# Performance work log

Measured on AMD Instinct MI355X. Metric: run time of the kernel, lower is better.

The kernel has to match this reference:

```python
import jax, jax.numpy as jnp
import numpy as np


def lstm_cell(carry, x, Wx, Wh, b):
    # carry = (h, c), x: [B, E]; standard fused-gate LSTM
    h, c = carry
    z = x @ Wx + h @ Wh + b  # [B, 4U]
    i, f, g, o = jnp.split(z, 4, axis=-1)
    c = jax.nn.sigmoid(f) * c + jax.nn.sigmoid(i) * jnp.tanh(g)
    h = jax.nn.sigmoid(o) * jnp.tanh(c)
    return (h, c)


def run_lstm(xs, Wx, Wh, b, units):
    # xs: [T, B, E] -> final hidden state [B, U]
    B = xs.shape[1]
    init = (jnp.zeros((B, units), xs.dtype), jnp.zeros((B, units), xs.dtype))
    def step(carry, x):
        carry = lstm_cell(carry, x, Wx, Wh, b)
        return carry, None
    (h, _), _ = jax.lax.scan(step, init, xs)
    return h


def setup_inputs() -> dict:
    key = jax.random.key(0)
    ks = jax.random.split(key, 12)
    B, T, V, E, U = 64, 512, 50000, 256, 512
    s = lambda *d: 1.0 / np.sqrt(d[0])
    return {
        "sentence": jax.random.randint(ks[0], (B, T), 0, V, dtype=jnp.int32),
        "emb": jax.random.normal(ks[1], (V, E), jnp.float32) * 0.02,
        "Wx_f": jax.random.normal(ks[2], (E, 4 * U), jnp.float32) * s(E),
        "Wh_f": jax.random.normal(ks[3], (U, 4 * U), jnp.float32) * s(U),
        "b_f": jnp.zeros((4 * U,), jnp.float32),
        "Wx_b": jax.random.normal(ks[4], (E, 4 * U), jnp.float32) * s(E),
        "Wh_b": jax.random.normal(ks[5], (U, 4 * U), jnp.float32) * s(U),
        "b_b": jnp.zeros((4 * U,), jnp.float32),
        "W1": jax.random.normal(ks[6], (2 * U, 64), jnp.float32) * s(2 * U),
        "b1": jnp.zeros((64,), jnp.float32),
        "W2": jax.random.normal(ks[7], (64, 1), jnp.float32) * s(64),
        "b2": jnp.zeros((1,), jnp.float32),
    }


def reference(sentence, emb, Wx_f, Wh_f, b_f, Wx_b, Wh_b, b_b, W1, b1, W2, b2):
    U = Wh_f.shape[0]
    x = emb[sentence]                      # [B, T, E]
    xs = jnp.swapaxes(x, 0, 1)             # [T, B, E]
    h_fwd = run_lstm(xs, Wx_f, Wh_f, b_f, U)           # forward direction
    h_bwd = run_lstm(xs[::-1], Wx_b, Wh_b, b_b, U)     # backward direction
    h = jnp.concatenate([h_fwd, h_bwd], axis=1)        # [B, 2U]
    hidden = h @ W1 + b1                    # Dense(64), linear
    return jax.nn.sigmoid(hidden @ W2 + b2) # Dense(1, sigmoid)
```

## Files before the change

kernel.cpp:

```cpp
#include <hip/hip_runtime.h>
#include <hip/hip_bf16.h>

typedef __bf16 bf16x8 __attribute__((ext_vector_type(8)));
typedef float f32x4 __attribute__((ext_vector_type(4)));
typedef unsigned int u32;
typedef unsigned short u16;
typedef unsigned long long u64;

#define T_ 512
#define E_ 256
#define U_ 512

static const size_t WS_XS = 0;
static const size_t WS_W2 = (size_t)16 << 20;
static const size_t WS_HP = WS_W2 + 6291456;
static const size_t WS_HF = WS_HP + 524288;

__device__ __forceinline__ float fsigm(float x) { return 1.f / (1.f + __expf(-x)); }
__device__ __forceinline__ float ftanh(float x) {
  float e = __expf(2.f * fabsf(x));
  float r = 1.f - 2.f / (e + 1.f);
  return copysignf(r, x);
}

__global__ void embed_swz_kernel(const int* __restrict__ sent,
                                 const float* __restrict__ emb,
                                 __bf16* __restrict__ xs_g) {
  int id = blockIdx.x * 256 + threadIdx.x;
  int gx = id & 31;
  int b  = (id >> 5) & 63;
  int t  = id >> 11;
  int idx = sent[b * T_ + t];
  const float* src = emb + (size_t)idx * E_ + gx * 8;
  bf16x8 v;
#pragma unroll
  for (int j = 0; j < 8; ++j) v[j] = (__bf16)src[j];
  int gs = gx ^ (b & 7);
  *(bf16x8*)(xs_g + (size_t)(t * 64 + b) * E_ + gs * 8) = v;
}

__global__ void __launch_bounds__(256)
wprep_kernel(const float* __restrict__ Wx_f, const float* __restrict__ Wh_f,
             const float* __restrict__ Wx_b, const float* __restrict__ Wh_b,
             __bf16* __restrict__ w2, u32* __restrict__ hpub) {
  int bid = blockIdx.x;
  int tid = threadIdx.x;
  {
    int zid = bid * 256 + tid;
    if (zid < 131072) hpub[zid] = 0u;
  }
  int jg = bid % 6;
  int wv = (bid / 6) & 7;
  int us = (bid / 48) & 15;
  int d  = bid / 768;
  int j    = jg * 4 + (tid >> 6);
  int lane = tid & 63;
  int c    = wv * 16 + (lane & 15);
  int ul   = c >> 2, gate = c & 3;
  int n    = gate * 512 + us * 32 + ul;
  int k0   = j * 32 + (lane >> 4) * 8;
  const float* Wx = d ? Wx_b : Wx_f;
  const float* Wh = d ? Wh_b : Wh_f;
  bf16x8 v;
#pragma unroll
  for (int e = 0; e < 8; ++e) {
    int k = k0 + e;
    float f = (k < 256) ? Wx[(size_t)k * 2048 + n] : Wh[(size_t)(k - 256) * 2048 + n];
    v[e] = (__bf16)f;
  }
  size_t og = ((size_t)((d * 16 + us) * 8 + wv) * 24 + j) * 64 + lane;
  *(bf16x8*)(w2 + og * 8) = v;
}

__global__ void __launch_bounds__(512)
lstm_main(const __bf16* __restrict__ xs_g, const __bf16* __restrict__ w2,
          u32* __restrict__ hpub, float* __restrict__ hfin,
          const float* __restrict__ b_f, const float* __restrict__ b_b) {
  __shared__ __align__(16) __bf16 xbuf[2][16 * 256];
  __shared__ __align__(16) __bf16 hbuf[16 * 512];

  const int wg   = blockIdx.x;
  const int dir  = wg >> 6;
  const int sl   = wg & 63;
  const int us   = sl >> 2;
  const int q    = sl & 3;
  const int tid  = threadIdx.x;
  const int wv   = tid >> 6;
  const int lane = tid & 63;
  const int bq_l = lane & 15;
  const int kq   = lane >> 4;
  const int bsw  = bq_l & 7;
  const int ul_own = wv * 4 + kq;
  const int u_own  = us * 32 + ul_own;
  const int b_own  = q * 16 + bq_l;

  bf16x8 wfrag[24];
  {
    const bf16x8* wp = (const bf16x8*)w2 +
                       ((size_t)((dir * 16 + us) * 8 + wv) * 24) * 64 + lane;
#pragma unroll
    for (int j = 0; j < 24; ++j) wfrag[j] = wp[j * 64];
  }

  const float* bias = dir ? b_b : b_f;
  const float bi  = bias[u_own];
  const float bff = bias[512 + u_own];
  const float bg  = bias[1024 + u_own];
  const float bo  = bias[1536 + u_own];
  float c_st = 0.f;

  u32* const pw0 = hpub + ((size_t)(dir * 2 + 0) * 64 + q * 16 + us) * 512 + wv * 64 + lane;
  u32* const pw1 = pw0 + 32768;

  const int us_p  = 2 * wv + (lane >> 5);
  const int lane5 = lane & 31;
  const u64* const cs0 = (const u64*)(hpub + ((size_t)(dir * 2 + 0) * 64 + q * 16 + us_p) * 512) + lane5;
  const u64* const cs1 = cs0 + 16384;
  const int cc = lane5 >> 3;
  const int cb0 = 2 * (lane5 & 7);
  const int cb1 = cb0 + 1;
  int cd0[8], cd1[8];
#pragma unroll
  for (int j = 0; j < 8; ++j) {
    int u = us_p * 32 + j * 4 + cc;
    int g = u >> 3;
    cd0[j] = cb0 * 1024 + ((g ^ (cb0 & 7)) << 4) + ((u & 7) << 1);
    cd1[j] = cb1 * 1024 + ((g ^ (cb1 & 7)) << 4) + ((u & 7) << 1);
  }

  {
    int t0 = dir ? (T_ - 1) : 0;
    const uint4* xsrc = (const uint4*)(xs_g + ((size_t)t0 * 64 + q * 16) * 256);
    ((uint4*)xbuf[0])[tid] = xsrc[tid];
  }
  __syncthreads();

  for (int t = 0;; ++t) {
    const bool lastt = (t == T_ - 1);
    u64 v[8];
    const u64* csrc = (t & 1) ? cs1 : cs0;
    if (t > 0) {
#pragma unroll
      for (int j = 0; j < 8; ++j)
        v[j] = __hip_atomic_load(csrc + j * 32, __ATOMIC_RELAXED, __HIP_MEMORY_SCOPE_AGENT);
    }
    uint4 xg;
    if (!lastt) {
      const int teff = dir ? (T_ - 2 - t) : (t + 1);
      xg = ((const uint4*)(xs_g + ((size_t)teff * 64 + q * 16) * 256))[tid];
    }

    f32x4 acc0 = {0.f, 0.f, 0.f, 0.f};
    f32x4 acc1 = {0.f, 0.f, 0.f, 0.f};
    const __bf16* xb = xbuf[t & 1];
#pragma unroll
    for (int j = 0; j < 8; ++j) {
      int g = j * 4 + kq;
      bf16x8 a = *(const bf16x8*)(xb + bq_l * 256 + ((g ^ bsw) << 3));
      if (j & 1) acc1 = __builtin_amdgcn_mfma_f32_16x16x32_bf16(wfrag[j], a, acc1, 0, 0, 0);
      else       acc0 = __builtin_amdgcn_mfma_f32_16x16x32_bf16(wfrag[j], a, acc0, 0, 0, 0);
    }

    if (t > 0) {
      const u32 ep = (u32)t;
      for (;;) {
        u32 bad = 0;
#pragma unroll
        for (int j = 0; j < 8; ++j)
          bad |= ((u32)v[j] ^ ep) | ((u32)(v[j] >> 32) ^ ep);
        bad &= 0xFFFFu;
        if (!__any((int)bad)) break;
        __builtin_amdgcn_s_sleep(1);
#pragma unroll
        for (int j = 0; j < 8; ++j)
          v[j] = __hip_atomic_load(csrc + j * 32, __ATOMIC_RELAXED, __HIP_MEMORY_SCOPE_AGENT);
      }
#pragma unroll
      for (int j = 0; j < 8; ++j) {
        *(u16*)((char*)hbuf + cd0[j]) = (u16)(v[j] >> 16);
        *(u16*)((char*)hbuf + cd1[j]) = (u16)(v[j] >> 48);
      }
      __syncthreads();
#pragma unroll
      for (int j = 0; j < 16; ++j) {
        int g = j * 4 + kq;
        bf16x8 a = *(const bf16x8*)(hbuf + bq_l * 512 + ((g ^ bsw) << 3));
        if (j & 1) acc1 = __builtin_amdgcn_mfma_f32_16x16x32_bf16(wfrag[8 + j], a, acc1, 0, 0, 0);
        else       acc0 = __builtin_amdgcn_mfma_f32_16x16x32_bf16(wfrag[8 + j], a, acc0, 0, 0, 0);
      }
    }

    const float zi = acc0[0] + acc1[0] + bi;
    const float zf = acc0[1] + acc1[1] + bff;
    const float zg = acc0[2] + acc1[2] + bg;
    const float zo = acc0[3] + acc1[3] + bo;
    c_st = fsigm(zf) * c_st + fsigm(zi) * ftanh(zg);
    const float hv = fsigm(zo) * ftanh(c_st);

    if (lastt) {
      hfin[(size_t)dir * 32768 + b_own * 512 + u_own] = hv;
      break;
    }

    {
      union { __bf16 h; u16 s; } cv;
      cv.h = (__bf16)hv;
      u32 word = ((u32)cv.s << 16) | (u32)(t + 1);
      __hip_atomic_store(((t + 1) & 1) ? pw1 : pw0, word, __ATOMIC_RELAXED,
                         __HIP_MEMORY_SCOPE_AGENT);
    }
    ((uint4*)xbuf[(t + 1) & 1])[tid] = xg;
    __syncthreads();
  }
}

__global__ void __launch_bounds__(1024)
dense_kernel(const float* __restrict__ hfin, const float* __restrict__ W1,
             const float* __restrict__ b1, const float* __restrict__ W2,
             const float* __restrict__ b2, float* __restrict__ out) {
  __shared__ float hid[64][64];
  const int t = threadIdx.x;
  const int b = t >> 4;
  const int jg = t & 15;
  float a0 = b1[jg * 4 + 0], a1 = b1[jg * 4 + 1], a2 = b1[jg * 4 + 2], a3 = b1[jg * 4 + 3];
#pragma unroll 8
  for (int k = 0; k < 1024; ++k) {
    const float hv = hfin[(size_t)(k >> 9) * 32768 + b * 512 + (k & 511)];
    const float4 w = *(const float4*)(W1 + (size_t)k * 64 + jg * 4);
    a0 += hv * w.x; a1 += hv * w.y; a2 += hv * w.z; a3 += hv * w.w;
  }
  hid[b][jg * 4 + 0] = a0; hid[b][jg * 4 + 1] = a1;
  hid[b][jg * 4 + 2] = a2; hid[b][jg * 4 + 3] = a3;
  __syncthreads();
  if (t < 64) {
    float l = b2[0];
#pragma unroll 8
    for (int j = 0; j < 64; ++j) l += hid[t][j] * W2[j];
    out[t] = 1.f / (1.f + __expf(-l));
  }
}

extern "C" void kernel_launch(void* const* d_in, const int* in_sizes, int n_in,
                              void* d_out, int out_size, void* d_ws, size_t ws_size,
                              hipStream_t stream) {
  const int*   sent = (const int*)d_in[0];
  const float* emb  = (const float*)d_in[1];
  const float* Wx_f = (const float*)d_in[2];
  const float* Wh_f = (const float*)d_in[3];
  const float* b_f  = (const float*)d_in[4];
  const float* Wx_b = (const float*)d_in[5];
  const float* Wh_b = (const float*)d_in[6];
  const float* b_b  = (const float*)d_in[7];
  const float* W1   = (const float*)d_in[8];
  const float* b1   = (const float*)d_in[9];
  const float* W2   = (const float*)d_in[10];
  const float* b2   = (const float*)d_in[11];
  float* out = (float*)d_out;

  char* ws = (char*)d_ws;
  __bf16* xs_g = (__bf16*)(ws + WS_XS);
  __bf16* w2   = (__bf16*)(ws + WS_W2);
  u32*    hpub = (u32*)(ws + WS_HP);
  float*  hfin = (float*)(ws + WS_HF);

  hipLaunchKernelGGL(embed_swz_kernel, dim3(4096), dim3(256), 0, stream, sent, emb, xs_g);
  hipLaunchKernelGGL(wprep_kernel, dim3(1536), dim3(256), 0, stream,
                     Wx_f, Wh_f, Wx_b, Wh_b, w2, hpub);

  void* args[] = {(void*)&xs_g, (void*)&w2, (void*)&hpub, (void*)&hfin,
                  (void*)&b_f, (void*)&b_b};
  hipLaunchCooperativeKernel((void*)lstm_main, dim3(128), dim3(512), args, 0, stream);

  hipLaunchKernelGGL(dense_kernel, dim3(1), dim3(1024), 0, stream,
                     hfin, W1, b1, W2, b2, out);
}
```

Measured before the change: 1.308 ms.

## Split LSTM recurrence over 256 smaller workgroups and hoist input projection

Re-partitions the persistent cooperative LSTM kernel from 128 workgroups of 512 threads to 256 workgroups of 256 threads, so each workgroup owns 16 hidden units instead of 32. The weight pre-layout and the h-publish buffer indexing change to match. The x-projection MFMAs for the next step now run right after the barrier, off the critical path that waits on h. The h gather is rewritten to pack four bf16 values per 64-bit LDS store. In exchange, each workgroup waits on more cross-workgroup flags per step, and twice as many workgroups take part in the grid-wide handshake.

```diff
diff --git a/kernel.cpp b/kernel.cpp
--- a/kernel.cpp
+++ b/kernel.cpp
@@ -50,14 +50,14 @@
     if (zid < 131072) hpub[zid] = 0u;
   }
   int jg = bid % 6;
-  int wv = (bid / 6) & 7;
-  int us = (bid / 48) & 15;
+  int wv = (bid / 6) & 3;
+  int us = (bid / 24) & 31;
   int d  = bid / 768;
   int j    = jg * 4 + (tid >> 6);
   int lane = tid & 63;
   int c    = wv * 16 + (lane & 15);
   int ul   = c >> 2, gate = c & 3;
-  int n    = gate * 512 + us * 32 + ul;
+  int n    = gate * 512 + us * 16 + ul;
   int k0   = j * 32 + (lane >> 4) * 8;
   const float* Wx = d ? Wx_b : Wx_f;
   const float* Wh = d ? Wh_b : Wh_f;
@@ -68,11 +68,11 @@
     float f = (k < 256) ? Wx[(size_t)k * 2048 + n] : Wh[(size_t)(k - 256) * 2048 + n];
     v[e] = (__bf16)f;
   }
-  size_t og = ((size_t)((d * 16 + us) * 8 + wv) * 24 + j) * 64 + lane;
+  size_t og = ((size_t)((d * 32 + us) * 4 + wv) * 24 + j) * 64 + lane;
   *(bf16x8*)(w2 + og * 8) = v;
 }
 
-__global__ void __launch_bounds__(512)
+__global__ void __launch_bounds__(256)
 lstm_main(const __bf16* __restrict__ xs_g, const __bf16* __restrict__ w2,
           u32* __restrict__ hpub, float* __restrict__ hfin,
           const float* __restrict__ b_f, const float* __restrict__ b_b) {
@@ -80,8 +80,8 @@
   __shared__ __align__(16) __bf16 hbuf[16 * 512];
 
   const int wg   = blockIdx.x;
-  const int dir  = wg >> 6;
-  const int sl   = wg & 63;
+  const int dir  = wg >> 7;
+  const int sl   = wg & 127;
   const int us   = sl >> 2;
   const int q    = sl & 3;
   const int tid  = threadIdx.x;
@@ -91,13 +91,13 @@
   const int kq   = lane >> 4;
   const int bsw  = bq_l & 7;
   const int ul_own = wv * 4 + kq;
-  const int u_own  = us * 32 + ul_own;
+  const int u_own  = us * 16 + ul_own;
   const int b_own  = q * 16 + bq_l;
 
   bf16x8 wfrag[24];
   {
     const bf16x8* wp = (const bf16x8*)w2 +
-                       ((size_t)((dir * 16 + us) * 8 + wv) * 24) * 64 + lane;
+                       ((size_t)((dir * 32 + us) * 4 + wv) * 24) * 64 + lane;
 #pragma unroll
     for (int j = 0; j < 24; ++j) wfrag[j] = wp[j * 64];
   }
@@ -109,76 +109,95 @@
   const float bo  = bias[1536 + u_own];
   float c_st = 0.f;
 
-  u32* const pw0 = hpub + ((size_t)(dir * 2 + 0) * 64 + q * 16 + us) * 512 + wv * 64 + lane;
+  u32* const pw0 = hpub + ((size_t)(dir * 2 + 0) * 4 + q) * 8192 + us * 256 + wv * 64 + lane;
   u32* const pw1 = pw0 + 32768;
 
-  const int us_p  = 2 * wv + (lane >> 5);
-  const int lane5 = lane & 31;
-  const u64* const cs0 = (const u64*)(hpub + ((size_t)(dir * 2 + 0) * 64 + q * 16 + us_p) * 512) + lane5;
-  const u64* const cs1 = cs0 + 16384;
-  const int cc = lane5 >> 3;
-  const int cb0 = 2 * (lane5 & 7);
-  const int cb1 = cb0 + 1;
-  int cd0[8], cd1[8];
-#pragma unroll
-  for (int j = 0; j < 8; ++j) {
-    int u = us_p * 32 + j * 4 + cc;
-    int g = u >> 3;
-    cd0[j] = cb0 * 1024 + ((g ^ (cb0 & 7)) << 4) + ((u & 7) << 1);
-    cd1[j] = cb1 * 1024 + ((g ^ (cb1 & 7)) << 4) + ((u & 7) << 1);
+  const int b2  = tid & 7;
+  const int u0  = ((tid >> 3) & 3) * 4;
+  const int ush = tid >> 5;
+  const u64* const cb = (const u64*)hpub + ((size_t)(dir * 2 + 0) * 4 + q) * 4096;
+  int cde[4], cdo[4];
+#pragma unroll
+  for (int J = 0; J < 4; ++J) {
+    int us_p = ush + 8 * J;
+    int ga   = us_p * 2 + (u0 >> 3);
+    int off  = (u0 & 7) * 2;
+    int b0   = 2 * b2, b1 = 2 * b2 + 1;
+    cde[J] = b0 * 1024 + ((ga ^ (b0 & 7)) << 4) + off;
+    cdo[J] = b1 * 1024 + ((ga ^ (b1 & 7)) << 4) + off;
   }
 
   {
     int t0 = dir ? (T_ - 1) : 0;
     const uint4* xsrc = (const uint4*)(xs_g + ((size_t)t0 * 64 + q * 16) * 256);
     ((uint4*)xbuf[0])[tid] = xsrc[tid];
+    ((uint4*)xbuf[0])[tid + 256] = xsrc[tid + 256];
   }
   __syncthreads();
+
+  f32x4 xacc0 = {0.f, 0.f, 0.f, 0.f};
+  f32x4 xacc1 = {0.f, 0.f, 0.f, 0.f};
+#pragma unroll
+  for (int j = 0; j < 8; ++j) {
+    int g = j * 4 + kq;
+    bf16x8 a = *(const bf16x8*)(xbuf[0] + bq_l * 256 + ((g ^ bsw) << 3));
+    if (j & 1) xacc1 = __builtin_amdgcn_mfma_f32_16x16x32_bf16(wfrag[j], a, xacc1, 0, 0, 0);
+    else       xacc0 = __builtin_amdgcn_mfma_f32_16x16x32_bf16(wfrag[j], a, xacc0, 0, 0, 0);
+  }
 
   for (int t = 0;; ++t) {
     const bool lastt = (t == T_ - 1);
-    u64 v[8];
-    const u64* csrc = (t & 1) ? cs1 : cs0;
+    u64 v[16];
+    const u64* csrc = cb + (size_t)(t & 1) * 16384;
     if (t > 0) {
 #pragma unroll
-      for (int j = 0; j < 8; ++j)
-        v[j] = __hip_atomic_load(csrc + j * 32, __ATOMIC_RELAXED, __HIP_MEMORY_SCOPE_AGENT);
-    }
-    uint4 xg;
+      for (int J = 0; J < 4; ++J)
+#pragma unroll
+        for (int du = 0; du < 4; ++du)
+          v[J * 4 + du] = __hip_atomic_load(
+              csrc + (ush + 8 * J) * 128 + (u0 + du) * 8 + b2,
+              __ATOMIC_RELAXED, __HIP_MEMORY_SCOPE_AGENT);
+    }
+    uint4 xg0, xg1;
     if (!lastt) {
       const int teff = dir ? (T_ - 2 - t) : (t + 1);
-      xg = ((const uint4*)(xs_g + ((size_t)teff * 64 + q * 16) * 256))[tid];
-    }
-
-    f32x4 acc0 = {0.f, 0.f, 0.f, 0.f};
-    f32x4 acc1 = {0.f, 0.f, 0.f, 0.f};
-    const __bf16* xb = xbuf[t & 1];
-#pragma unroll
-    for (int j = 0; j < 8; ++j) {
-      int g = j * 4 + kq;
-      bf16x8 a = *(const bf16x8*)(xb + bq_l * 256 + ((g ^ bsw) << 3));
-      if (j & 1) acc1 = __builtin_amdgcn_mfma_f32_16x16x32_bf16(wfrag[j], a, acc1, 0, 0, 0);
-      else       acc0 = __builtin_amdgcn_mfma_f32_16x16x32_bf16(wfrag[j], a, acc0, 0, 0, 0);
-    }
+      const uint4* xsrc = (const uint4*)(xs_g + ((size_t)teff * 64 + q * 16) * 256);
+      xg0 = xsrc[tid];
+      xg1 = xsrc[tid + 256];
+    }
+
+    f32x4 acc0 = xacc0;
+    f32x4 acc1 = xacc1;
 
     if (t > 0) {
       const u32 ep = (u32)t;
       for (;;) {
         u32 bad = 0;
 #pragma unroll
-        for (int j = 0; j < 8; ++j)
+        for (int j = 0; j < 16; ++j)
           bad |= ((u32)v[j] ^ ep) | ((u32)(v[j] >> 32) ^ ep);
         bad &= 0xFFFFu;
         if (!__any((int)bad)) break;
         __builtin_amdgcn_s_sleep(1);
 #pragma unroll
-        for (int j = 0; j < 8; ++j)
-          v[j] = __hip_atomic_load(csrc + j * 32, __ATOMIC_RELAXED, __HIP_MEMORY_SCOPE_AGENT);
+        for (int J = 0; J < 4; ++J)
+#pragma unroll
+          for (int du = 0; du < 4; ++du)
+            v[J * 4 + du] = __hip_atomic_load(
+                csrc + (ush + 8 * J) * 128 + (u0 + du) * 8 + b2,
+                __ATOMIC_RELAXED, __HIP_MEMORY_SCOPE_AGENT);
       }
 #pragma unroll
-      for (int j = 0; j < 8; ++j) {
-        *(u16*)((char*)hbuf + cd0[j]) = (u16)(v[j] >> 16);
-        *(u16*)((char*)hbuf + cd1[j]) = (u16)(v[j] >> 48);
+      for (int J = 0; J < 4; ++J) {
+        u64 we = 0, wo = 0;
+#pragma unroll
+        for (int du = 0; du < 4; ++du) {
+          u64 x = v[J * 4 + du];
+          we |= (u64)((u32)(x >> 16) & 0xFFFFu) << (16 * du);
+          wo |= (u64)((u32)(x >> 48) & 0xFFFFu) << (16 * du);
+        }
+        *(u64*)((char*)hbuf + cde[J]) = we;
+        *(u64*)((char*)hbuf + cdo[J]) = wo;
       }
       __syncthreads();
 #pragma unroll
@@ -209,8 +228,23 @@
       __hip_atomic_store(((t + 1) & 1) ? pw1 : pw0, word, __ATOMIC_RELAXED,
                          __HIP_MEMORY_SCOPE_AGENT);
     }
-    ((uint4*)xbuf[(t + 1) & 1])[tid] = xg;
+    {
+      uint4* xdst = (uint4*)xbuf[(t + 1) & 1];
+      xdst[tid] = xg0;
+      xdst[tid + 256] = xg1;
+    }
     __syncthreads();
+
+    xacc0 = (f32x4){0.f, 0.f, 0.f, 0.f};
+    xacc1 = (f32x4){0.f, 0.f, 0.f, 0.f};
+    const __bf16* xb = xbuf[(t + 1) & 1];
+#pragma unroll
+    for (int j = 0; j < 8; ++j) {
+      int g = j * 4 + kq;
+      bf16x8 a = *(const bf16x8*)(xb + bq_l * 256 + ((g ^ bsw) << 3));
+      if (j & 1) xacc1 = __builtin_amdgcn_mfma_f32_16x16x32_bf16(wfrag[j], a, xacc1, 0, 0, 0);
+      else       xacc0 = __builtin_amdgcn_mfma_f32_16x16x32_bf16(wfrag[j], a, xacc0, 0, 0, 0);
+    }
   }
 }
 
@@ -269,7 +303,7 @@
 
   void* args[] = {(void*)&xs_g, (void*)&w2, (void*)&hpub, (void*)&hfin,
                   (void*)&b_f, (void*)&b_b};
-  hipLaunchCooperativeKernel((void*)lstm_main, dim3(128), dim3(512), args, 0, stream);
+  hipLaunchCooperativeKernel((void*)lstm_main, dim3(256), dim3(256), args, 0, stream);
 
   hipLaunchKernelGGL(dense_kernel, dim3(1), dim3(1024), 0, stream,
                      hfin, W1, b1, W2, b2, out);
```

Result: slower. 1.358 ms (+3.8%).

## Halve LSTM workgroups, give each wave two column tiles, split h exchange into halves

Applied to the files above, without the earlier changes.

Each workgroup now owns 64 hidden units instead of 32, so the cooperative launch drops from 128 to 64 workgroups and every wave keeps 48 weight fragments in registers across two column tiles. The h exchange is restructured: loads are packed into 64-bit LDS stores, and the recurrent matmul is split into two halves, so work on the first half of h can start before the second half has been published. The aim is to cut the cross-workgroup synchronisation cost and overlap communication with MFMA work. The cost is higher register pressure (48 fragments plus more accumulators) under launch_bounds(512,2), a risk of spilling, and more serial compute per step.

```diff
diff --git a/kernel.cpp b/kernel.cpp
--- a/kernel.cpp
+++ b/kernel.cpp
@@ -50,14 +50,17 @@
     if (zid < 131072) hpub[zid] = 0u;
   }
   int jg = bid % 6;
-  int wv = (bid / 6) & 7;
-  int us = (bid / 48) & 15;
+  int ct = (bid / 6) & 1;
+  int wv = (bid / 12) & 7;
+  int us = (bid / 96) & 7;
   int d  = bid / 768;
   int j    = jg * 4 + (tid >> 6);
   int lane = tid & 63;
-  int c    = wv * 16 + (lane & 15);
-  int ul   = c >> 2, gate = c & 3;
-  int n    = gate * 512 + us * 32 + ul;
+  int r    = lane & 15;
+  int tile = wv * 2 + ct;
+  int ul   = tile * 4 + (r >> 2);
+  int gate = r & 3;
+  int n    = gate * 512 + us * 64 + ul;
   int k0   = j * 32 + (lane >> 4) * 8;
   const float* Wx = d ? Wx_b : Wx_f;
   const float* Wh = d ? Wh_b : Wh_f;
@@ -68,11 +71,11 @@
     float f = (k < 256) ? Wx[(size_t)k * 2048 + n] : Wh[(size_t)(k - 256) * 2048 + n];
     v[e] = (__bf16)f;
   }
-  size_t og = ((size_t)((d * 16 + us) * 8 + wv) * 24 + j) * 64 + lane;
+  size_t og = ((size_t)(((d * 8 + us) * 8 + wv) * 2 + ct) * 24 + j) * 64 + lane;
   *(bf16x8*)(w2 + og * 8) = v;
 }
 
-__global__ void __launch_bounds__(512)
+__global__ void __launch_bounds__(512, 2)
 lstm_main(const __bf16* __restrict__ xs_g, const __bf16* __restrict__ w2,
           u32* __restrict__ hpub, float* __restrict__ hfin,
           const float* __restrict__ b_f, const float* __restrict__ b_b) {
@@ -80,8 +83,8 @@
   __shared__ __align__(16) __bf16 hbuf[16 * 512];
 
   const int wg   = blockIdx.x;
-  const int dir  = wg >> 6;
-  const int sl   = wg & 63;
+  const int dir  = wg >> 5;
+  const int sl   = wg & 31;
   const int us   = sl >> 2;
   const int q    = sl & 3;
   const int tid  = threadIdx.x;
@@ -90,42 +93,46 @@
   const int bq_l = lane & 15;
   const int kq   = lane >> 4;
   const int bsw  = bq_l & 7;
-  const int ul_own = wv * 4 + kq;
-  const int u_own  = us * 32 + ul_own;
   const int b_own  = q * 16 + bq_l;
 
-  bf16x8 wfrag[24];
+  bf16x8 wfrag[48];
   {
     const bf16x8* wp = (const bf16x8*)w2 +
-                       ((size_t)((dir * 16 + us) * 8 + wv) * 24) * 64 + lane;
-#pragma unroll
-    for (int j = 0; j < 24; ++j) wfrag[j] = wp[j * 64];
+                       ((size_t)((dir * 8 + us) * 8 + wv) * 48) * 64 + lane;
+#pragma unroll
+    for (int j = 0; j < 48; ++j) wfrag[j] = wp[j * 64];
   }
 
   const float* bias = dir ? b_b : b_f;
-  const float bi  = bias[u_own];
-  const float bff = bias[512 + u_own];
-  const float bg  = bias[1024 + u_own];
-  const float bo  = bias[1536 + u_own];
-  float c_st = 0.f;
-
-  u32* const pw0 = hpub + ((size_t)(dir * 2 + 0) * 64 + q * 16 + us) * 512 + wv * 64 + lane;
-  u32* const pw1 = pw0 + 32768;
-
-  const int us_p  = 2 * wv + (lane >> 5);
-  const int lane5 = lane & 31;
-  const u64* const cs0 = (const u64*)(hpub + ((size_t)(dir * 2 + 0) * 64 + q * 16 + us_p) * 512) + lane5;
-  const u64* const cs1 = cs0 + 16384;
-  const int cc = lane5 >> 3;
-  const int cb0 = 2 * (lane5 & 7);
-  const int cb1 = cb0 + 1;
-  int cd0[8], cd1[8];
-#pragma unroll
-  for (int j = 0; j < 8; ++j) {
-    int u = us_p * 32 + j * 4 + cc;
-    int g = u >> 3;
-    cd0[j] = cb0 * 1024 + ((g ^ (cb0 & 7)) << 4) + ((u & 7) << 1);
-    cd1[j] = cb1 * 1024 + ((g ^ (cb1 & 7)) << 4) + ((u & 7) << 1);
+  float bi[2], bff[2], bg[2], bo[2], c_st[2];
+  int u_own[2];
+#pragma unroll
+  for (int ct = 0; ct < 2; ++ct) {
+    u_own[ct] = us * 64 + (wv * 2 + ct) * 4 + kq;
+    bi[ct]  = bias[u_own[ct]];
+    bff[ct] = bias[512 + u_own[ct]];
+    bg[ct]  = bias[1024 + u_own[ct]];
+    bo[ct]  = bias[1536 + u_own[ct]];
+    c_st[ct] = 0.f;
+  }
+
+  u32* const pw0 = hpub + ((size_t)(dir * 2 + 0) * 4 + q) * 8192 +
+                   us * 1024 + wv * 128 + lane;
+
+  const int ph   = tid >> 7;
+  const int inr  = tid & 127;
+  const int b2   = inr & 7;
+  const int u0g  = inr >> 3;
+  const int u0   = u0g * 4;
+  const u64* const cb = (const u64*)hpub + ((size_t)(dir * 2 + 0) * 4 + q) * 4096;
+  const int be = 2 * b2, bo_ = 2 * b2 + 1;
+  int cde[2], cdo[2];
+#pragma unroll
+  for (int H = 0; H < 2; ++H) {
+    int g0  = (H * 4 + ph) * 8 + (u0g >> 1);
+    int off = (u0g & 1) * 8;
+    cde[H] = be  * 1024 + ((g0 ^ (be  & 7)) << 4) + off;
+    cdo[H] = bo_ * 1024 + ((g0 ^ (bo_ & 7)) << 4) + off;
   }
 
   {
@@ -138,11 +145,15 @@
   for (int t = 0;; ++t) {
     const bool lastt = (t == T_ - 1);
     u64 v[8];
-    const u64* csrc = (t & 1) ? cs1 : cs0;
+    const u64* csrc = cb + (size_t)(t & 1) * 16384;
     if (t > 0) {
 #pragma unroll
-      for (int j = 0; j < 8; ++j)
-        v[j] = __hip_atomic_load(csrc + j * 32, __ATOMIC_RELAXED, __HIP_MEMORY_SCOPE_AGENT);
+      for (int H = 0; H < 2; ++H)
+#pragma unroll
+        for (int du = 0; du < 4; ++du)
+          v[H * 4 + du] = __hip_atomic_load(
+              csrc + (H * 4 + ph) * 512 + (u0 + du) * 8 + b2,
+              __ATOMIC_RELAXED, __HIP_MEMORY_SCOPE_AGENT);
     }
     uint4 xg;
     if (!lastt) {
@@ -150,15 +161,24 @@
       xg = ((const uint4*)(xs_g + ((size_t)teff * 64 + q * 16) * 256))[tid];
     }
 
-    f32x4 acc0 = {0.f, 0.f, 0.f, 0.f};
-    f32x4 acc1 = {0.f, 0.f, 0.f, 0.f};
+    f32x4 acc0[2], acc1[2];
+#pragma unroll
+    for (int ct = 0; ct < 2; ++ct) {
+      acc0[ct] = (f32x4){0.f, 0.f, 0.f, 0.f};
+      acc1[ct] = (f32x4){0.f, 0.f, 0.f, 0.f};
+    }
     const __bf16* xb = xbuf[t & 1];
 #pragma unroll
     for (int j = 0; j < 8; ++j) {
       int g = j * 4 + kq;
       bf16x8 a = *(const bf16x8*)(xb + bq_l * 256 + ((g ^ bsw) << 3));
-      if (j & 1) acc1 = __builtin_amdgcn_mfma_f32_16x16x32_bf16(wfrag[j], a, acc1, 0, 0, 0);
-      else       acc0 = __builtin_amdgcn_mfma_f32_16x16x32_bf16(wfrag[j], a, acc0, 0, 0, 0);
+      if (j & 1) {
+        acc1[0] = __builtin_amdgcn_mfma_f32_16x16x32_bf16(wfrag[j], a, acc1[0], 0, 0, 0);
+        acc1[1] = __builtin_amdgcn_mfma_f32_16x16x32_bf16(wfrag[24 + j], a, acc1[1], 0, 0, 0);
+      } else {
+        acc0[0] = __builtin_amdgcn_mfma_f32_16x16x32_bf16(wfrag[j], a, acc0[0], 0, 0, 0);
+        acc0[1] = __builtin_amdgcn_mfma_f32_16x16x32_bf16(wfrag[24 + j], a, acc0[1], 0, 0, 0);
+      }
     }
 
     if (t > 0) {
@@ -166,49 +186,99 @@
       for (;;) {
         u32 bad = 0;
 #pragma unroll
-        for (int j = 0; j < 8; ++j)
+        for (int j = 0; j < 4; ++j)
           bad |= ((u32)v[j] ^ ep) | ((u32)(v[j] >> 32) ^ ep);
         bad &= 0xFFFFu;
         if (!__any((int)bad)) break;
         __builtin_amdgcn_s_sleep(1);
 #pragma unroll
-        for (int j = 0; j < 8; ++j)
-          v[j] = __hip_atomic_load(csrc + j * 32, __ATOMIC_RELAXED, __HIP_MEMORY_SCOPE_AGENT);
-      }
+        for (int du = 0; du < 4; ++du)
+          v[du] = __hip_atomic_load(csrc + ph * 512 + (u0 + du) * 8 + b2,
+                                    __ATOMIC_RELAXED, __HIP_MEMORY_SCOPE_AGENT);
+      }
+      {
+        u64 we = 0, wo = 0;
+#pragma unroll
+        for (int du = 0; du < 4; ++du) {
+          u64 x = v[du];
+          we |= (u64)((u32)(x >> 16) & 0xFFFFu) << (16 * du);
+          wo |= (u64)((u32)(x >> 48) & 0xFFFFu) << (16 * du);
+        }
+        *(u64*)((char*)hbuf + cde[0]) = we;
+        *(u64*)((char*)hbuf + cdo[0]) = wo;
+      }
+      __syncthreads();
 #pragma unroll
       for (int j = 0; j < 8; ++j) {
-        *(u16*)((char*)hbuf + cd0[j]) = (u16)(v[j] >> 16);
-        *(u16*)((char*)hbuf + cd1[j]) = (u16)(v[j] >> 48);
-      }
-      __syncthreads();
-#pragma unroll
-      for (int j = 0; j < 16; ++j) {
         int g = j * 4 + kq;
         bf16x8 a = *(const bf16x8*)(hbuf + bq_l * 512 + ((g ^ bsw) << 3));
-        if (j & 1) acc1 = __builtin_amdgcn_mfma_f32_16x16x32_bf16(wfrag[8 + j], a, acc1, 0, 0, 0);
-        else       acc0 = __builtin_amdgcn_mfma_f32_16x16x32_bf16(wfrag[8 + j], a, acc0, 0, 0, 0);
-      }
-    }
-
-    const float zi = acc0[0] + acc1[0] + bi;
-    const float zf = acc0[1] + acc1[1] + bff;
-    const float zg = acc0[2] + acc1[2] + bg;
-    const float zo = acc0[3] + acc1[3] + bo;
-    c_st = fsigm(zf) * c_st + fsigm(zi) * ftanh(zg);
-    const float hv = fsigm(zo) * ftanh(c_st);
-
-    if (lastt) {
-      hfin[(size_t)dir * 32768 + b_own * 512 + u_own] = hv;
-      break;
-    }
-
-    {
-      union { __bf16 h; u16 s; } cv;
-      cv.h = (__bf16)hv;
-      u32 word = ((u32)cv.s << 16) | (u32)(t + 1);
-      __hip_atomic_store(((t + 1) & 1) ? pw1 : pw0, word, __ATOMIC_RELAXED,
-                         __HIP_MEMORY_SCOPE_AGENT);
-    }
+        if (j & 1) {
+          acc1[0] = __builtin_amdgcn_mfma_f32_16x16x32_bf16(wfrag[8 + j], a, acc1[0], 0, 0, 0);
+          acc1[1] = __builtin_amdgcn_mfma_f32_16x16x32_bf16(wfrag[32 + j], a, acc1[1], 0, 0, 0);
+        } else {
+          acc0[0] = __builtin_amdgcn_mfma_f32_16x16x32_bf16(wfrag[8 + j], a, acc0[0], 0, 0, 0);
+          acc0[1] = __builtin_amdgcn_mfma_f32_16x16x32_bf16(wfrag[32 + j], a, acc0[1], 0, 0, 0);
+        }
+      }
+      for (;;) {
+        u32 bad = 0;
+#pragma unroll
+        for (int j = 4; j < 8; ++j)
+          bad |= ((u32)v[j] ^ ep) | ((u32)(v[j] >> 32) ^ ep);
+        bad &= 0xFFFFu;
+        if (!__any((int)bad)) break;
+        __builtin_amdgcn_s_sleep(1);
+#pragma unroll
+        for (int du = 0; du < 4; ++du)
+          v[4 + du] = __hip_atomic_load(csrc + (4 + ph) * 512 + (u0 + du) * 8 + b2,
+                                        __ATOMIC_RELAXED, __HIP_MEMORY_SCOPE_AGENT);
+      }
+      {
+        u64 we = 0, wo = 0;
+#pragma unroll
+        for (int du = 0; du < 4; ++du) {
+          u64 x = v[4 + du];
+          we |= (u64)((u32)(x >> 16) & 0xFFFFu) << (16 * du);
+          wo |= (u64)((u32)(x >> 48) & 0xFFFFu) << (16 * du);
+        }
+        *(u64*)((char*)hbuf + cde[1]) = we;
+        *(u64*)((char*)hbuf + cdo[1]) = wo;
+      }
+      __syncthreads();
+#pragma unroll
+      for (int j = 8; j < 16; ++j) {
+        int g = j * 4 + kq;
+        bf16x8 a = *(const bf16x8*)(hbuf + bq_l * 512 + ((g ^ bsw) << 3));
+        if (j & 1) {
+          acc1[0] = __builtin_amdgcn_mfma_f32_16x16x32_bf16(wfrag[8 + j], a, acc1[0], 0, 0, 0);
+          acc1[1] = __builtin_amdgcn_mfma_f32_16x16x32_bf16(wfrag[32 + j], a, acc1[1], 0, 0, 0);
+        } else {
+          acc0[0] = __builtin_amdgcn_mfma_f32_16x16x32_bf16(wfrag[8 + j], a, acc0[0], 0, 0, 0);
+          acc0[1] = __builtin_amdgcn_mfma_f32_16x16x32_bf16(wfrag[32 + j], a, acc0[1], 0, 0, 0);
+        }
+      }
+    }
+
+#pragma unroll
+    for (int ct = 0; ct < 2; ++ct) {
+      const float zi = acc0[ct][0] + acc1[ct][0] + bi[ct];
+      const float zf = acc0[ct][1] + acc1[ct][1] + bff[ct];
+      const float zg = acc0[ct][2] + acc1[ct][2] + bg[ct];
+      const float zo = acc0[ct][3] + acc1[ct][3] + bo[ct];
+      c_st[ct] = fsigm(zf) * c_st[ct] + fsigm(zi) * ftanh(zg);
+      const float hv = fsigm(zo) * ftanh(c_st[ct]);
+      if (lastt) {
+        hfin[(size_t)dir * 32768 + b_own * 512 + u_own[ct]] = hv;
+      } else {
+        union { __bf16 h; u16 s; } cv;
+        cv.h = (__bf16)hv;
+        u32 word = ((u32)cv.s << 16) | (u32)(t + 1);
+        __hip_atomic_store(pw0 + ((t + 1) & 1) * 32768 + ct * 64, word,
+                           __ATOMIC_RELAXED, __HIP_MEMORY_SCOPE_AGENT);
+      }
+    }
+    if (lastt) break;
+
     ((uint4*)xbuf[(t + 1) & 1])[tid] = xg;
     __syncthreads();
   }
@@ -269,7 +339,7 @@
 
   void* args[] = {(void*)&xs_g, (void*)&w2, (void*)&hpub, (void*)&hfin,
                   (void*)&b_f, (void*)&b_b};
-  hipLaunchCooperativeKernel((void*)lstm_main, dim3(128), dim3(512), args, 0, stream);
+  hipLaunchCooperativeKernel((void*)lstm_main, dim3(64), dim3(512), args, 0, stream);
 
   hipLaunchKernelGGL(dense_kernel, dim3(1), dim3(1024), 0, stream,
                      hfin, W1, b1, W2, b2, out);
```

Result: slower. 2.763 ms (+111.2%).

## Merge per-step barriers via 4-deep x buffering and double-buffered h tile

Applied to the files above, without the earlier changes.

The x input ring in LDS grows from two slots to four, and x is now prefetched two steps ahead. The h staging buffer is double-buffered. Together these let each timestep use a single workgroup barrier instead of two, which targets the sync latency on the serial recurrence path. The cost is more LDS and extra register live ranges for the prefetched x vector.

```diff
diff --git a/kernel.cpp b/kernel.cpp
--- a/kernel.cpp
+++ b/kernel.cpp
@@ -76,8 +76,8 @@
 lstm_main(const __bf16* __restrict__ xs_g, const __bf16* __restrict__ w2,
           u32* __restrict__ hpub, float* __restrict__ hfin,
           const float* __restrict__ b_f, const float* __restrict__ b_b) {
-  __shared__ __align__(16) __bf16 xbuf[2][16 * 256];
-  __shared__ __align__(16) __bf16 hbuf[16 * 512];
+  __shared__ __align__(16) __bf16 xbuf[4][16 * 256];
+  __shared__ __align__(16) __bf16 hbuf[2][16 * 512];
 
   const int wg   = blockIdx.x;
   const int dir  = wg >> 6;
@@ -109,12 +109,12 @@
   const float bo  = bias[1536 + u_own];
   float c_st = 0.f;
 
-  u32* const pw0 = hpub + ((size_t)(dir * 2 + 0) * 64 + q * 16 + us) * 512 + wv * 64 + lane;
-  u32* const pw1 = pw0 + 32768;
+  u32* const pw0 = hpub + ((size_t)((dir * 2 + 0) * 64 + q * 16 + us)) * 512 +
+                   wv * 64 + lane;
 
   const int us_p  = 2 * wv + (lane >> 5);
   const int lane5 = lane & 31;
-  const u64* const cs0 = (const u64*)(hpub + ((size_t)(dir * 2 + 0) * 64 + q * 16 + us_p) * 512) + lane5;
+  const u64* const cs0 = (const u64*)(hpub + ((size_t)((dir * 2 + 0) * 64 + q * 16 + us_p)) * 512) + lane5;
   const u64* const cs1 = cs0 + 16384;
   const int cc = lane5 >> 3;
   const int cb0 = 2 * (lane5 & 7);
@@ -129,11 +129,17 @@
   }
 
   {
-    int t0 = dir ? (T_ - 1) : 0;
-    const uint4* xsrc = (const uint4*)(xs_g + ((size_t)t0 * 64 + q * 16) * 256);
-    ((uint4*)xbuf[0])[tid] = xsrc[tid];
+    int te0 = dir ? (T_ - 1) : 0;
+    int te1 = dir ? (T_ - 2) : 1;
+    ((uint4*)xbuf[0])[tid] = ((const uint4*)(xs_g + ((size_t)te0 * 64 + q * 16) * 256))[tid];
+    ((uint4*)xbuf[1])[tid] = ((const uint4*)(xs_g + ((size_t)te1 * 64 + q * 16) * 256))[tid];
   }
   __syncthreads();
+  uint4 xg;
+  {
+    int te2 = dir ? (T_ - 3) : 2;
+    xg = ((const uint4*)(xs_g + ((size_t)te2 * 64 + q * 16) * 256))[tid];
+  }
 
   for (int t = 0;; ++t) {
     const bool lastt = (t == T_ - 1);
@@ -144,15 +150,10 @@
       for (int j = 0; j < 8; ++j)
         v[j] = __hip_atomic_load(csrc + j * 32, __ATOMIC_RELAXED, __HIP_MEMORY_SCOPE_AGENT);
     }
-    uint4 xg;
-    if (!lastt) {
-      const int teff = dir ? (T_ - 2 - t) : (t + 1);
-      xg = ((const uint4*)(xs_g + ((size_t)teff * 64 + q * 16) * 256))[tid];
-    }
 
     f32x4 acc0 = {0.f, 0.f, 0.f, 0.f};
     f32x4 acc1 = {0.f, 0.f, 0.f, 0.f};
-    const __bf16* xb = xbuf[t & 1];
+    const __bf16* xb = xbuf[t & 3];
 #pragma unroll
     for (int j = 0; j < 8; ++j) {
       int g = j * 4 + kq;
@@ -161,6 +162,13 @@
       else       acc0 = __builtin_amdgcn_mfma_f32_16x16x32_bf16(wfrag[j], a, acc0, 0, 0, 0);
     }
 
+    ((uint4*)xbuf[(t + 2) & 3])[tid] = xg;
+    {
+      int tn = (t + 3 < T_) ? (t + 3) : (T_ - 1);
+      int te = dir ? (T_ - 1 - tn) : tn;
+      xg = ((const uint4*)(xs_g + ((size_t)te * 64 + q * 16) * 256))[tid];
+    }
+
     if (t > 0) {
       const u32 ep = (u32)t;
       for (;;) {
@@ -175,16 +183,25 @@
         for (int j = 0; j < 8; ++j)
           v[j] = __hip_atomic_load(csrc + j * 32, __ATOMIC_RELAXED, __HIP_MEMORY_SCOPE_AGENT);
       }
+      char* hb = (char*)hbuf[t & 1];
 #pragma unroll
       for (int j = 0; j < 8; ++j) {
-        *(u16*)((char*)hbuf + cd0[j]) = (u16)(v[j] >> 16);
-        *(u16*)((char*)hbuf + cd1[j]) = (u16)(v[j] >> 48);
+        *(u16*)(hb + cd0[j]) = (u16)(v[j] >> 16);
+        *(u16*)(hb + cd1[j]) = (u16)(v[j] >> 48);
       }
-      __syncthreads();
+    }
+
+    asm volatile("s_waitcnt lgkmcnt(0)" ::: "memory");
+    __builtin_amdgcn_sched_barrier(0);
+    __builtin_amdgcn_s_barrier();
+    __builtin_amdgcn_sched_barrier(0);
+
+    if (t > 0) {
+      const __bf16* hb = hbuf[t & 1];
 #pragma unroll
       for (int j = 0; j < 16; ++j) {
         int g = j * 4 + kq;
-        bf16x8 a = *(const bf16x8*)(hbuf + bq_l * 512 + ((g ^ bsw) << 3));
+        bf16x8 a = *(const bf16x8*)(hb + bq_l * 512 + ((g ^ bsw) << 3));
         if (j & 1) acc1 = __builtin_amdgcn_mfma_f32_16x16x32_bf16(wfrag[8 + j], a, acc1, 0, 0, 0);
         else       acc0 = __builtin_amdgcn_mfma_f32_16x16x32_bf16(wfrag[8 + j], a, acc0, 0, 0, 0);
       }
@@ -206,11 +223,9 @@
       union { __bf16 h; u16 s; } cv;
       cv.h = (__bf16)hv;
       u32 word = ((u32)cv.s << 16) | (u32)(t + 1);
-      __hip_atomic_store(((t + 1) & 1) ? pw1 : pw0, word, __ATOMIC_RELAXED,
+      __hip_atomic_store(pw0 + ((t + 1) & 1) * 32768, word, __ATOMIC_RELAXED,
                          __HIP_MEMORY_SCOPE_AGENT);
     }
-    ((uint4*)xbuf[(t + 1) & 1])[tid] = xg;
-    __syncthreads();
   }
 }
 
```

New measurement: 1.620 ms. 1.24x slower.
